# Kernel optimization log

Hardware: AMD Instinct MI355X
Metric: run time of the kernel (lower is better)

## Reference

```python
import jax, jax.numpy as jnp
import numpy as np

EPS = 0.01                      # cfg.eps
INV_4PI = 1.0 / (4.0 * np.pi)   # 3D free-space Green's constant


def setup_inputs() -> dict:
    key = jax.random.key(0)
    k1, k2, k3 = jax.random.split(key, 3)
    B, M, d = 32768, 2048, 3
    return {
        "x_query": jax.random.normal(k1, (B, d), dtype=jnp.float32),
        "x_land": jax.random.normal(k2, (M, d), dtype=jnp.float32),
        "g_land": jax.random.normal(k3, (M,), dtype=jnp.float32),
    }


def reference(x_query, x_land, g_land):
    # Regularized 3D Poisson Green's function:
    #   G(x,y)      =  1/(4*pi) * (||x-y||^2 + eps^2)^(-1/2)
    #   grad_x G    = -1/(4*pi) * (x-y) * (||x-y||^2 + eps^2)^(-3/2)
    M = x_land.shape[0]
    r2 = (jnp.sum(x_query * x_query, axis=1)[:, None]
          - 2.0 * (x_query @ x_land.T)
          + jnp.sum(x_land * x_land, axis=1)[None, :])
    t = jnp.maximum(r2, 0.0) + EPS * EPS          # (B, M), regularized
    G = INV_4PI * jax.lax.rsqrt(t)                # (B, M)
    v_hat = (G * g_land[None, :]).sum(axis=1) / M # (B,)
    # fused gradient reduction: avoid materializing (B, M, d) dG.
    # sum_m g_m * dG = -1/(4pi) * [ x_q * sum_m c_m  -  c @ x_land ],
    # where c_m = g_m * t^(-3/2)
    c = g_land[None, :] * t ** (-1.5)             # (B, M)
    gradv_hat = -INV_4PI * (x_query * c.sum(axis=1, keepdims=True) - c @ x_land) / M
    return v_hat, gradv_hat
```

## Files before the change

### kernel.cpp

```cpp
#include <hip/hip_runtime.h>
#include <math.h>


#define EPS2    1e-4f
#define INV_4PI 0.07957747154594767f

constexpr int M_LAND = 2048;
constexpr int NW     = 16;
constexpr int SLICE  = M_LAND / NW;
constexpr int QPB    = 128;

typedef float f32x2 __attribute__((ext_vector_type(2)));

__global__ __launch_bounds__(1024, 4)
void poisson_r7_kernel(const float* __restrict__ xq,
                       const float* __restrict__ xl,
                       const float* __restrict__ gl,
                       float* __restrict__ out, int B)
{
    __shared__ float4 pack[M_LAND];
    __shared__ float  part[NW][QPB][5];

    const int tid = threadIdx.x;
    for (int j = tid; j < M_LAND; j += 1024)
        pack[j] = make_float4(xl[3*j], xl[3*j+1], xl[3*j+2], gl[j]);

    const int lane  = tid & 63;
    const int w     = tid >> 6;
    const int qbase = blockIdx.x * QPB;
    const int qa    = qbase + lane;
    const int qb    = qbase + 64 + lane;

    const float a0 = xq[3*qa], a1 = xq[3*qa+1], a2 = xq[3*qa+2];
    const float b0 = xq[3*qb], b1 = xq[3*qb+1], b2 = xq[3*qb+2];

    f32x2 Qn0 = {-2.0f*a0, -2.0f*b0};
    f32x2 Qn1 = {-2.0f*a1, -2.0f*b1};
    f32x2 Qn2 = {-2.0f*a2, -2.0f*b2};
    f32x2 QE  = {a0*a0 + a1*a1 + a2*a2, b0*b0 + b1*b1 + b2*b2};

    float av_a=0.f, ac_a=0.f, ax_a=0.f, ay_a=0.f, az_a=0.f;
    float av_b=0.f, ac_b=0.f, ax_b=0.f, ay_b=0.f, az_b=0.f;

    __syncthreads();

    const int base = w * SLICE;
#pragma unroll 8
    for (int i = 0; i < SLICE; ++i) {
        const float4 p = pack[base + i];
        f32x2 P01 = {p.x, p.y};
        f32x2 P2G = {p.z, p.w};

        float n2 = fmaf(p.x, p.x, fmaf(p.y, p.y, fmaf(p.z, p.z, EPS2)));

        f32x2 T;
        asm("v_pk_fma_f32 %0, %1, %2, %3 op_sel:[0,0,0] op_sel_hi:[0,1,1]\n\t"
            "v_pk_fma_f32 %0, %4, %5, %0 op_sel:[1,0,0] op_sel_hi:[1,1,1]\n\t"
            "v_pk_fma_f32 %0, %4, %6, %0 op_sel:[0,0,0] op_sel_hi:[0,1,1]"
            : "=&v"(T)
            : "v"(P2G), "v"(Qn2), "v"(QE), "v"(P01), "v"(Qn1), "v"(Qn0));

        float ta = fmaxf(T.x + n2, EPS2);
        float tb = fmaxf(T.y + n2, EPS2);
        float sa = __builtin_amdgcn_rsqf(ta);
        float sb = __builtin_amdgcn_rsqf(tb);

        float s3a = sa * sa * sa;
        float s3b = sb * sb * sb;
        float ca  = p.w * s3a;
        float cb  = p.w * s3b;

        av_a = fmaf(p.w, sa, av_a);   av_b = fmaf(p.w, sb, av_b);
        ac_a += ca;                   ac_b += cb;
        ax_a = fmaf(ca, p.x, ax_a);   ax_b = fmaf(cb, p.x, ax_b);
        ay_a = fmaf(ca, p.y, ay_a);   ay_b = fmaf(cb, p.y, ay_b);
        az_a = fmaf(ca, p.z, az_a);   az_b = fmaf(cb, p.z, az_b);
    }

    part[w][lane][0] = av_a;  part[w][lane][1] = ac_a;
    part[w][lane][2] = ax_a;  part[w][lane][3] = ay_a;  part[w][lane][4] = az_a;
    part[w][lane+64][0] = av_b;  part[w][lane+64][1] = ac_b;
    part[w][lane+64][2] = ax_b;  part[w][lane+64][3] = ay_b;  part[w][lane+64][4] = az_b;

    __syncthreads();

    if (tid < 512) {
        const int q   = tid >> 2;
        const int cmp = tid & 3;
        const int qg  = qbase + q;
        if (cmp == 0) {
            float s = 0.f;
            #pragma unroll
            for (int ww = 0; ww < NW; ++ww) s += part[ww][q][0];
            out[qg] = s * (INV_4PI / (float)M_LAND);
        } else {
            float sc = 0.f, sy = 0.f;
            #pragma unroll
            for (int ww = 0; ww < NW; ++ww) {
                sc += part[ww][q][1];
                sy += part[ww][q][1 + cmp];
            }
            const float qc = xq[3*qg + (cmp-1)];
            out[B + 3*qg + (cmp-1)] =
                (-INV_4PI / (float)M_LAND) * fmaf(qc, sc, -sy);
        }
    }
}

extern "C" void kernel_launch(void* const* d_in, const int* in_sizes, int n_in,
                              void* d_out, int out_size, void* d_ws, size_t ws_size,
                              hipStream_t stream)
{
    const float* xq = (const float*)d_in[0];
    const float* xl = (const float*)d_in[1];
    const float* gl = (const float*)d_in[2];
    float* out = (float*)d_out;

    const int B    = in_sizes[0] / 3;
    const int grid = B / QPB;

    poisson_r7_kernel<<<grid, 1024, 0, stream>>>(xq, xl, gl, out, B);
}
```

Baseline: 31.22 us.

## Assign one query per wavefront with landmark-parallel lanes and shuffle reduction

Replaces the shared-memory tiled kernel, where each lane handled two queries and waves split the landmarks, with a layout where each wavefront owns one query and its 64 lanes stride over all landmarks read from global/L2. A separate pre-pass kernel writes a packed per-landmark record (-2*x, |x|^2+eps^2) into the workspace. Partial sums are combined with a cross-lane xor-shuffle reduction instead of an LDS reduction. This drops LDS staging and the block barriers, but adds a second launch, 5x6 shuffle rounds per query, and repeated global loads of the landmark data per wave. The packed v_pk_fma path is also lost.

```diff
diff --git a/kernel.cpp b/kernel.cpp
--- a/kernel.cpp
+++ b/kernel.cpp
@@ -6,104 +6,79 @@
 #define INV_4PI 0.07957747154594767f
 
 constexpr int M_LAND = 2048;
-constexpr int NW     = 16;
-constexpr int SLICE  = M_LAND / NW;
-constexpr int QPB    = 128;
+constexpr int ITERS  = M_LAND / 64;
 
-typedef float f32x2 __attribute__((ext_vector_type(2)));
+__global__ void poisson_pack_kernel(const float* __restrict__ xl,
+                                    float* __restrict__ rec)
+{
+    int j = blockIdx.x * 256 + threadIdx.x;
+    if (j < M_LAND) {
+        float l0 = xl[3*j], l1 = xl[3*j+1], l2 = xl[3*j+2];
+        ((float4*)rec)[j] =
+            make_float4(-2.0f*l0, -2.0f*l1, -2.0f*l2,
+                        l0*l0 + l1*l1 + l2*l2 + EPS2);
+    }
+}
 
-__global__ __launch_bounds__(1024, 4)
-void poisson_r7_kernel(const float* __restrict__ xq,
-                       const float* __restrict__ xl,
-                       const float* __restrict__ gl,
-                       float* __restrict__ out, int B)
+template<bool PACKED>
+__global__ __launch_bounds__(512)
+void poisson_qwave_kernel(const float* __restrict__ xq,
+                          const float* __restrict__ rec,
+                          const float* __restrict__ gl,
+                          float* __restrict__ out, int B)
 {
-    __shared__ float4 pack[M_LAND];
-    __shared__ float  part[NW][QPB][5];
+    const int lane = threadIdx.x & 63;
+    const int wid  = __builtin_amdgcn_readfirstlane(threadIdx.x >> 6);
+    const int q    = blockIdx.x * 8 + wid;
+    if (q >= B) return;
 
-    const int tid = threadIdx.x;
-    for (int j = tid; j < M_LAND; j += 1024)
-        pack[j] = make_float4(xl[3*j], xl[3*j+1], xl[3*j+2], gl[j]);
+    const float q0 = xq[3*q], q1 = xq[3*q+1], q2 = xq[3*q+2];
+    const float qe = q0*q0 + q1*q1 + q2*q2;
 
-    const int lane  = tid & 63;
-    const int w     = tid >> 6;
-    const int qbase = blockIdx.x * QPB;
-    const int qa    = qbase + lane;
-    const int qb    = qbase + 64 + lane;
+    float av = 0.f, ac = 0.f, ax = 0.f, ay = 0.f, az = 0.f;
 
-    const float a0 = xq[3*qa], a1 = xq[3*qa+1], a2 = xq[3*qa+2];
-    const float b0 = xq[3*qb], b1 = xq[3*qb+1], b2 = xq[3*qb+2];
+#pragma unroll 4
+    for (int it = 0; it < ITERS; ++it) {
+        const int j = it * 64 + lane;
+        float m0, m1, m2, ne;
+        if (PACKED) {
+            const float4 r = ((const float4*)rec)[j];
+            m0 = r.x; m1 = r.y; m2 = r.z; ne = r.w;
+        } else {
+            float l0 = rec[3*j], l1 = rec[3*j+1], l2 = rec[3*j+2];
+            m0 = -2.0f*l0; m1 = -2.0f*l1; m2 = -2.0f*l2;
+            ne = l0*l0 + l1*l1 + l2*l2 + EPS2;
+        }
+        const float g = gl[j];
 
-    f32x2 Qn0 = {-2.0f*a0, -2.0f*b0};
-    f32x2 Qn1 = {-2.0f*a1, -2.0f*b1};
-    f32x2 Qn2 = {-2.0f*a2, -2.0f*b2};
-    f32x2 QE  = {a0*a0 + a1*a1 + a2*a2, b0*b0 + b1*b1 + b2*b2};
+        float t = fmaf(m0, q0, fmaf(m1, q1, fmaf(m2, q2, qe + ne)));
+        t = fmaxf(t, EPS2);
+        float s  = __builtin_amdgcn_rsqf(t);
+        float s3 = s * s * s;
+        float c  = g * s3;
 
-    float av_a=0.f, ac_a=0.f, ax_a=0.f, ay_a=0.f, az_a=0.f;
-    float av_b=0.f, ac_b=0.f, ax_b=0.f, ay_b=0.f, az_b=0.f;
-
-    __syncthreads();
-
-    const int base = w * SLICE;
-#pragma unroll 8
-    for (int i = 0; i < SLICE; ++i) {
-        const float4 p = pack[base + i];
-        f32x2 P01 = {p.x, p.y};
-        f32x2 P2G = {p.z, p.w};
-
-        float n2 = fmaf(p.x, p.x, fmaf(p.y, p.y, fmaf(p.z, p.z, EPS2)));
-
-        f32x2 T;
-        asm("v_pk_fma_f32 %0, %1, %2, %3 op_sel:[0,0,0] op_sel_hi:[0,1,1]\n\t"
-            "v_pk_fma_f32 %0, %4, %5, %0 op_sel:[1,0,0] op_sel_hi:[1,1,1]\n\t"
-            "v_pk_fma_f32 %0, %4, %6, %0 op_sel:[0,0,0] op_sel_hi:[0,1,1]"
-            : "=&v"(T)
-            : "v"(P2G), "v"(Qn2), "v"(QE), "v"(P01), "v"(Qn1), "v"(Qn0));
-
-        float ta = fmaxf(T.x + n2, EPS2);
-        float tb = fmaxf(T.y + n2, EPS2);
-        float sa = __builtin_amdgcn_rsqf(ta);
-        float sb = __builtin_amdgcn_rsqf(tb);
-
-        float s3a = sa * sa * sa;
-        float s3b = sb * sb * sb;
-        float ca  = p.w * s3a;
-        float cb  = p.w * s3b;
-
-        av_a = fmaf(p.w, sa, av_a);   av_b = fmaf(p.w, sb, av_b);
-        ac_a += ca;                   ac_b += cb;
-        ax_a = fmaf(ca, p.x, ax_a);   ax_b = fmaf(cb, p.x, ax_b);
-        ay_a = fmaf(ca, p.y, ay_a);   ay_b = fmaf(cb, p.y, ay_b);
-        az_a = fmaf(ca, p.z, az_a);   az_b = fmaf(cb, p.z, az_b);
+        av = fmaf(g, s, av);
+        ac += c;
+        ax = fmaf(c, m0, ax);
+        ay = fmaf(c, m1, ay);
+        az = fmaf(c, m2, az);
     }
 
-    part[w][lane][0] = av_a;  part[w][lane][1] = ac_a;
-    part[w][lane][2] = ax_a;  part[w][lane][3] = ay_a;  part[w][lane][4] = az_a;
-    part[w][lane+64][0] = av_b;  part[w][lane+64][1] = ac_b;
-    part[w][lane+64][2] = ax_b;  part[w][lane+64][3] = ay_b;  part[w][lane+64][4] = az_b;
+#pragma unroll
+    for (int m = 1; m < 64; m <<= 1) {
+        av += __shfl_xor(av, m, 64);
+        ac += __shfl_xor(ac, m, 64);
+        ax += __shfl_xor(ax, m, 64);
+        ay += __shfl_xor(ay, m, 64);
+        az += __shfl_xor(az, m, 64);
+    }
 
-    __syncthreads();
-
-    if (tid < 512) {
-        const int q   = tid >> 2;
-        const int cmp = tid & 3;
-        const int qg  = qbase + q;
-        if (cmp == 0) {
-            float s = 0.f;
-            #pragma unroll
-            for (int ww = 0; ww < NW; ++ww) s += part[ww][q][0];
-            out[qg] = s * (INV_4PI / (float)M_LAND);
-        } else {
-            float sc = 0.f, sy = 0.f;
-            #pragma unroll
-            for (int ww = 0; ww < NW; ++ww) {
-                sc += part[ww][q][1];
-                sy += part[ww][q][1 + cmp];
-            }
-            const float qc = xq[3*qg + (cmp-1)];
-            out[B + 3*qg + (cmp-1)] =
-                (-INV_4PI / (float)M_LAND) * fmaf(qc, sc, -sy);
-        }
+    if (lane == 0) {
+        const float k = INV_4PI / (float)M_LAND;
+        out[q] = av * k;
+        out[B + 3*q + 0] = -k * fmaf(q0, ac, 0.5f * ax);
+        out[B + 3*q + 1] = -k * fmaf(q1, ac, 0.5f * ay);
+        out[B + 3*q + 2] = -k * fmaf(q2, ac, 0.5f * az);
     }
 }
 
@@ -117,7 +92,13 @@
     float* out = (float*)d_out;
 
     const int B    = in_sizes[0] / 3;
-    const int grid = B / QPB;
+    const int grid = (B + 7) / 8;
 
-    poisson_r7_kernel<<<grid, 1024, 0, stream>>>(xq, xl, gl, out, B);
+    if (ws_size >= (size_t)(M_LAND * 4 * sizeof(float))) {
+        float* rec = (float*)d_ws;
+        poisson_pack_kernel<<<(M_LAND + 255) / 256, 256, 0, stream>>>(xl, rec);
+        poisson_qwave_kernel<true><<<grid, 512, 0, stream>>>(xq, rec, gl, out, B);
+    } else {
+        poisson_qwave_kernel<false><<<grid, 512, 0, stream>>>(xq, xl, gl, out, B);
+    }
 }
```

After: 48.34 us. +54.8%, slower.
